# Kernel tuning notes

Measured on AMD Instinct MI355X. Metric: run time of the kernel, lower is better.

The kernel has to match this reference:

```python
import jax, jax.numpy as jnp
import numpy as np

B, N, C, H = 4, 1025, 768, 12
KEEP_RATIO = 0.25
BETA = 1.0


def setup_inputs() -> dict:
    key = jax.random.key(0)
    k1, k2, k3, k4, k5 = jax.random.split(key, 5)
    x = jax.random.normal(k1, (B, N, C), dtype=jnp.float32)
    ucb_count_score = jax.random.uniform(k2, (H, N), dtype=jnp.float32)
    W_qkv = jax.random.normal(k3, (C, 3 * C), dtype=jnp.float32) * 0.02
    W_proj = jax.random.normal(k4, (C, C), dtype=jnp.float32) * 0.02
    b_proj = jax.random.normal(k5, (C,), dtype=jnp.float32) * 0.02
    return {"x": x, "ucb_count_score": ucb_count_score, "W_qkv": W_qkv,
            "W_proj": W_proj, "b_proj": b_proj, "counter": 100, "ucb_enabled": 1}


def reference(x, ucb_count_score, W_qkv, W_proj, b_proj, counter, ucb_enabled):
    Bn, Nn, Cn = x.shape
    Dh = Cn // H
    scale = Dh ** -0.5
    # qkv projection (no bias, qkv_bias=False)
    qkv = (x @ W_qkv).reshape(Bn, Nn, 3, H, Dh)
    q = jnp.transpose(qkv[:, :, 0], (0, 2, 1, 3))  # [B,H,N,Dh]
    k = jnp.transpose(qkv[:, :, 1], (0, 2, 1, 3))
    v = jnp.transpose(qkv[:, :, 2], (0, 2, 1, 3))
    attn_probs = jax.nn.softmax(jnp.einsum('bhnd,bhmd->bhnm', q, k) * scale, axis=-1)

    if ucb_enabled and counter > 50:
        # UCB pruning path (exclude_cls=True, keep_ratio set)
        total_patches = Nn - 1
        k_sel = max(1, int(total_patches * KEEP_RATIO))
        patch_scores = attn_probs[:, :, :, 1:].mean(axis=2)  # [B,H,N-1]
        expl = BETA * jnp.sqrt(jnp.log(counter + 1.0) / (ucb_count_score[:, 1:] + 1e-6))  # [H,N-1]
        global_ucb = (patch_scores + expl[None]).mean(axis=1)  # [B,N-1]
        _, sel = jax.lax.top_k(global_ucb, k_sel)  # [B,k]
        tok = sel + 1  # shift for CLS
        # keep[b,j] = 1 if token j is CLS or selected in batch b
        keep = jnp.zeros((Bn, Nn), dtype=attn_probs.dtype)
        keep = keep.at[jnp.arange(Bn)[:, None], tok].set(1.0).at[:, 0].set(1.0)
        # mask[b,h,i,j] = keep[b,i] OR keep[b,j]
        mask = jnp.maximum(keep[:, None, :, None], keep[:, None, None, :])
        pruned = attn_probs * mask
        pruned = pruned / (pruned.sum(axis=-1, keepdims=True) + 1e-8)
        context = jnp.einsum('bhnm,bhmd->bhnd', pruned, v)
        cnt = jnp.zeros((Nn,), dtype=jnp.float32).at[tok.reshape(-1)].add(1.0) / Bn
        score_delta = jnp.broadcast_to(cnt[None, :], ucb_count_score.shape)
    else:
        context = jnp.einsum('bhnm,bhmd->bhnd', attn_probs, v)
        score_delta = None

    out = context.transpose(0, 2, 1, 3).reshape(Bn, Nn, Cn) @ W_proj + b_proj
    return out, score_delta
```

## Files before the change

### kernel.cpp

```cpp
#include <hip/hip_runtime.h>
#include <hip/hip_bf16.h>
#include <math.h>

#define Bb 4
#define Nn 1025
#define Cc 768
#define Hh 12
#define BH (Bb*Hh)
#define M_ROWS 4100
#define KSEL 256
#define JP 1152
#define IT_TILES 68
#define NIB 17
#define NIB32 33
#define NSW 9
#define MT16 264
#define KC24 24
#define JT16 72
#define JS32 36
#define ESTR 1160
#define NPART 396
#define QSCALE 0.18033688011112042f

typedef __attribute__((ext_vector_type(8))) short short8;
typedef __attribute__((ext_vector_type(4))) float floatx4;

static __device__ inline unsigned short f2bf(float v) {
    __hip_bfloat16 b = __float2bfloat16(v);
    return *reinterpret_cast<unsigned short*>(&b);
}
static __device__ inline unsigned short tbf(float f) {
    union { float f; unsigned u; } x; x.f = f;
    return (unsigned short)(x.u >> 16);
}
static __device__ inline float fexp2(float x) {
    return __builtin_amdgcn_exp2f(x);
}
static __device__ inline float bflo(unsigned u) {
    return __uint_as_float((u & 0xffffu) << 16);
}
static __device__ inline float bfhi(unsigned u) {
    return __uint_as_float(u & 0xffff0000u);
}

static __device__ inline void async16(const unsigned short* g, unsigned short* l) {
    __builtin_amdgcn_global_load_lds(
        (const __attribute__((address_space(1))) unsigned int*)g,
        (__attribute__((address_space(3))) unsigned int*)l, 16, 0, 0);
}

__global__ void zero_ws(unsigned int* p, int n) {
    for (int i = blockIdx.x * 256 + threadIdx.x; i < n; i += gridDim.x * 256)
        p[i] = 0u;
}

__global__ __launch_bounds__(256)
void cast_x(const float* __restrict__ x, unsigned short* __restrict__ xA) {
    int s = blockIdx.x * 256 + threadIdx.x;
    int ml = s & 15, q = (s >> 4) & 3;
    int t2 = s >> 6;
    int mt = t2 % MT16, kc = t2 / MT16;
    int m = mt * 16 + ml, k = kc * 32 + q * 8;
    uint4 pk = {0u, 0u, 0u, 0u};
    if (m < M_ROWS) {
        float4 a = *(const float4*)&x[(size_t)m * 768 + k];
        float4 b2 = *(const float4*)&x[(size_t)m * 768 + k + 4];
        pk.x = (unsigned)f2bf(a.x)  | ((unsigned)f2bf(a.y)  << 16);
        pk.y = (unsigned)f2bf(a.z)  | ((unsigned)f2bf(a.w)  << 16);
        pk.z = (unsigned)f2bf(b2.x) | ((unsigned)f2bf(b2.y) << 16);
        pk.w = (unsigned)f2bf(b2.z) | ((unsigned)f2bf(b2.w) << 16);
    }
    *(uint4*)&xA[(size_t)s * 8] = pk;
}

__global__ __launch_bounds__(256)
void cast_w(const float* __restrict__ W, unsigned short* __restrict__ WB,
            int N, int NT) {
    int s = blockIdx.x * 256 + threadIdx.x;
    int nl = s & 15, q = (s >> 4) & 3;
    int t2 = s >> 6;
    int nt = t2 % NT, kc = t2 / NT;
    int n = nt * 16 + nl, k = kc * 32 + q * 8;
    unsigned hv[8];
#pragma unroll
    for (int e = 0; e < 8; ++e)
        hv[e] = f2bf(W[(size_t)(k + e) * N + n]);
    uint4 pk;
    pk.x = hv[0] | (hv[1] << 16);
    pk.y = hv[2] | (hv[3] << 16);
    pk.z = hv[4] | (hv[5] << 16);
    pk.w = hv[6] | (hv[7] << 16);
    *(uint4*)&WB[(size_t)s * 8] = pk;
}

__global__ __launch_bounds__(256, 2)
void gemm_mfma(const unsigned short* __restrict__ Af,
               const unsigned short* __restrict__ Bf,
               int Nt16, int mode,
               unsigned short* __restrict__ qB, unsigned short* __restrict__ kF,
               unsigned short* __restrict__ vF,
               float* __restrict__ outp, const float* __restrict__ bias)
{
    __shared__ __align__(16) unsigned short ldsA[4096];
    __shared__ __align__(16) unsigned short ldsB[4096];
    const int tid = threadIdx.x;
    const int ln = tid & 63, w = tid >> 6;
    const int wm = w >> 1, wn = w & 1;
    const int mb = blockIdx.x, nb = blockIdx.y;

    floatx4 acc[4][4];
#pragma unroll
    for (int mt = 0; mt < 4; ++mt)
#pragma unroll
        for (int nt = 0; nt < 4; ++nt)
            acc[mt][nt] = (floatx4){0.f, 0.f, 0.f, 0.f};

    for (int kc = 0; kc < KC24; ++kc) {
        const unsigned short* gA = Af + ((size_t)(kc * MT16 + mb * 8)) * 512;
        const unsigned short* gB = Bf + ((size_t)(kc * Nt16 + nb * 8)) * 512;
        async16(gA + (size_t)(w * 128 + ln) * 8,      &ldsA[w * 1024]);
        async16(gA + (size_t)(w * 128 + 64 + ln) * 8, &ldsA[w * 1024 + 512]);
        async16(gB + (size_t)(w * 128 + ln) * 8,      &ldsB[w * 1024]);
        async16(gB + (size_t)(w * 128 + 64 + ln) * 8, &ldsB[w * 1024 + 512]);
        __syncthreads();

        short8 Am[4], Bn[4];
#pragma unroll
        for (int mt = 0; mt < 4; ++mt)
            Am[mt] = *(const short8*)&ldsA[((wm * 4 + mt) * 64 + ln) * 8];
#pragma unroll
        for (int nt = 0; nt < 4; ++nt)
            Bn[nt] = *(const short8*)&ldsB[((wn * 4 + nt) * 64 + ln) * 8];
#pragma unroll
        for (int mt = 0; mt < 4; ++mt)
#pragma unroll
            for (int nt = 0; nt < 4; ++nt)
                acc[mt][nt] = __builtin_amdgcn_mfma_f32_16x16x32_bf16(
                    Am[mt], Bn[nt], acc[mt][nt], 0, 0, 0);
        __syncthreads();
    }

    const int q = ln >> 4, l15 = ln & 15;
    if (mode == 1) {
#pragma unroll
        for (int nt = 0; nt < 4; ++nt) {
            int gn = nb * 128 + wn * 64 + nt * 16 + l15;
            float bv = bias[gn];
#pragma unroll
            for (int mt = 0; mt < 4; ++mt) {
                int gmb = mb * 128 + wm * 64 + mt * 16 + q * 4;
#pragma unroll
                for (int r = 0; r < 4; ++r) {
                    int gm = gmb + r;
                    if (gm < M_ROWS)
                        outp[(size_t)gm * 768 + gn] = acc[mt][nt][r] + bv;
                }
            }
        }
    } else {
#pragma unroll
        for (int nt = 0; nt < 4; ++nt) {
            int gn = nb * 128 + wn * 64 + nt * 16 + l15;
            int s = (gn >= 1536) ? 2 : (gn >= 768 ? 1 : 0);
            int rr = gn - s * Cc;
            int h = rr >> 6, d = rr & 63;
#pragma unroll
            for (int mt = 0; mt < 4; ++mt) {
                int gmb = mb * 128 + wm * 64 + mt * 16 + q * 4;
#pragma unroll
                for (int r = 0; r < 4; ++r) {
                    int gm = gmb + r;
                    if (gm >= M_ROWS) continue;
                    int b = gm / Nn;
                    int n = gm - b * Nn;
                    int bh = b * Hh + h;
                    float val = acc[mt][nt][r];
                    if (s == 0) {
                        int idx = (((bh * IT_TILES + (n >> 4)) * 2 + (d >> 5)) * 512)
                                  + ((((d & 31) >> 3) * 16 + (n & 15)) * 8) + (d & 7);
                        qB[idx] = f2bf(val * QSCALE);
                    } else if (s == 1) {
                        size_t idx = ((((size_t)bh * JT16 + (n >> 4)) * 2 + (d >> 5)) * 64
                                      + ((d >> 3) & 3) * 16 + (n & 15)) * 8 + (d & 7);
                        kF[idx] = f2bf(val);
                    } else {
                        size_t idx = ((((size_t)bh * JS32 + (n >> 5)) * 4 + (d >> 4)) * 64
                                      + ((n >> 3) & 3) * 16 + (d & 15)) * 8 + (n & 7);
                        vF[idx] = f2bf(val);
                    }
                }
            }
        }
    }
}

__global__ __launch_bounds__(256, 2)
void attn_colsum_mfma(const unsigned short* __restrict__ qB,
                      const unsigned short* __restrict__ kF,
                      float* __restrict__ colsum_part)
{
    __shared__ unsigned short expS[32 * ESTR];
    __shared__ float red16[16][32];
    __shared__ float linv[32];

    const int blk = blockIdx.x;
    const int x8 = blk & 7, g = blk >> 3;
    const int bh = x8 * 6 + (g % 6);
    const int ib = g / 6;
    const int tid = threadIdx.x;
    const int ws = tid >> 6;
    const int ln = tid & 63;
    const int i16 = ln & 15, q = ln >> 4;

    const unsigned short* kBase = kF + (size_t)bh * JT16 * 1024;

    short8 Qf[2][2];
#pragma unroll
    for (int it = 0; it < 2; ++it)
#pragma unroll
        for (int kc = 0; kc < 2; ++kc)
            Qf[it][kc] = *(const short8*)&qB[(((size_t)bh * IT_TILES + ib * 2 + it) * 2 + kc) * 512 + ln * 8];

    float lacc[2][2] = {{0.f, 0.f}, {0.f, 0.f}};

    short8 Kc[2][2], Kn[2][2];
#pragma unroll
    for (int jt = 0; jt < 2; ++jt)
#pragma unroll
        for (int kc = 0; kc < 2; ++kc)
            Kc[jt][kc] = *(const short8*)&kBase[(((ws * 2 + jt) * 2 + kc) * 64 + ln) * 8];

    for (int sw = 0; sw < NSW; ++sw) {
        if (sw + 1 < NSW) {
#pragma unroll
            for (int jt = 0; jt < 2; ++jt)
#pragma unroll
                for (int kc = 0; kc < 2; ++kc)
                    Kn[jt][kc] = *(const short8*)&kBase[((((sw + 1) * 8 + ws * 2 + jt) * 2 + kc) * 64 + ln) * 8];
        }

        floatx4 S[2][2];
#pragma unroll
        for (int it = 0; it < 2; ++it)
#pragma unroll
            for (int jt = 0; jt < 2; ++jt) {
                S[it][jt] = (floatx4){0.f, 0.f, 0.f, 0.f};
#pragma unroll
                for (int kc = 0; kc < 2; ++kc)
                    S[it][jt] = __builtin_amdgcn_mfma_f32_16x16x32_bf16(Kc[jt][kc], Qf[it][kc], S[it][jt], 0, 0, 0);
            }

        const int jbase0 = sw * 128 + ws * 32 + q * 4;
#pragma unroll
        for (int it = 0; it < 2; ++it) {
            const int irow = it * 16 + i16;
#pragma unroll
            for (int jt = 0; jt < 2; ++jt) {
                int jbase = jbase0 + jt * 16;
                float p[4];
#pragma unroll
                for (int r = 0; r < 4; ++r) {
                    float vld = (jbase + r < Nn) ? 1.f : 0.f;
                    p[r] = fexp2(S[it][jt][r]) * vld;
                }
                lacc[it][jt] += (p[0] + p[1]) + (p[2] + p[3]);
                uint2 pk;
                pk.x = (unsigned)tbf(p[0]) | ((unsigned)tbf(p[1]) << 16);
                pk.y = (unsigned)tbf(p[2]) | ((unsigned)tbf(p[3]) << 16);
                *(uint2*)&expS[irow * ESTR + jbase] = pk;
            }
        }
#pragma unroll
        for (int jt = 0; jt < 2; ++jt)
#pragma unroll
            for (int kc = 0; kc < 2; ++kc)
                Kc[jt][kc] = Kn[jt][kc];
    }

    __syncthreads();
#pragma unroll
    for (int it = 0; it < 2; ++it)
        red16[ws * 4 + q][it * 16 + i16] = lacc[it][0] + lacc[it][1];
    __syncthreads();
    if (tid < 32) {
        float s = 0.f;
#pragma unroll
        for (int t = 0; t < 16; ++t) s += red16[t][tid];
        int gi = ib * 32 + tid;
        linv[tid] = (gi < Nn) ? 1.f / s : 0.f;
    }
    __syncthreads();

    float* prow = colsum_part + (size_t)(bh * NIB32 + ib) * JP;
    for (int grp = tid; grp < 288; grp += 256) {
        int j0 = grp * 4;
        float a0 = 0.f, a1 = 0.f, a2 = 0.f, a3 = 0.f;
#pragma unroll 8
        for (int i = 0; i < 32; ++i) {
            uint2 v = *(const uint2*)&expS[i * ESTR + j0];
            float li = linv[i];
            a0 += bflo(v.x) * li;
            a1 += bfhi(v.x) * li;
            a2 += bflo(v.y) * li;
            a3 += bfhi(v.y) * li;
        }
        float4 o = {a0, a1, a2, a3};
        *(float4*)&prow[j0] = o;
    }
}

__global__ __launch_bounds__(1024)
void ucb_topk(const float* __restrict__ colsum_part, const float* __restrict__ ucb_score,
              const int* __restrict__ counter_p,
              float* __restrict__ keepP, float* __restrict__ cnt)
{
    const int b = blockIdx.x;
    const int tid = threadIdx.x;
    __shared__ float vals[1024];
    __shared__ int   idxs[1024];

    const int j = tid + 1;
    const float* pb = colsum_part + (size_t)b * NPART * JP + j;
    float c0 = 0.f, c1 = 0.f, c2 = 0.f, c3 = 0.f;
#pragma unroll 4
    for (int g2 = 0; g2 < NPART; g2 += 4) {
        c0 += pb[(size_t)(g2 + 0) * JP];
        c1 += pb[(size_t)(g2 + 1) * JP];
        c2 += pb[(size_t)(g2 + 2) * JP];
        c3 += pb[(size_t)(g2 + 3) * JP];
    }
    float cs = (c0 + c1) + (c2 + c3);

    float lc = logf((float)(*counter_p) + 1.0f);
    float s = cs * (1.0f / (float)Nn);
#pragma unroll
    for (int h = 0; h < Hh; ++h)
        s += sqrtf(lc / (ucb_score[h * Nn + j] + 1e-6f));
    s *= (1.0f / (float)Hh);
    vals[tid] = s; idxs[tid] = tid;
    __syncthreads();

    for (int k = 2; k <= 1024; k <<= 1) {
        for (int jj = k >> 1; jj > 0; jj >>= 1) {
            int partner = tid ^ jj;
            if (partner > tid) {
                float v1 = vals[tid], v2 = vals[partner];
                int i1 = idxs[tid], i2 = idxs[partner];
                bool gt = (v1 > v2) || (v1 == v2 && i1 < i2);
                bool desc = ((tid & k) == 0);
                if (desc ? !gt : gt) {
                    vals[tid] = v2; vals[partner] = v1;
                    idxs[tid] = i2; idxs[partner] = i1;
                }
            }
            __syncthreads();
        }
    }

    if (tid < KSEL) {
        int tok = idxs[tid] + 1;
        keepP[b * JP + tok] = 1.f;
        atomicAdd(&cnt[tok], 1.0f / (float)Bb);
    }
    if (tid == 0) keepP[b * JP + 0] = 1.f;
}

__global__ void write_delta(const float* __restrict__ cnt, float* __restrict__ out2) {
    int t = blockIdx.x * 256 + threadIdx.x;
    if (t < Hh * Nn) out2[t] = cnt[t % Nn];
}

__global__ __launch_bounds__(256, 2)
void attn_ctx_mfma(const unsigned short* __restrict__ qB,
                   const unsigned short* __restrict__ kF,
                   const unsigned short* __restrict__ vF,
                   const float* __restrict__ keepP, unsigned short* __restrict__ ctxA)
{
    __shared__ __align__(16) char smem[29440];
    unsigned short* Pall = (unsigned short*)smem;
    float* red16 = (float*)(smem + 20480);
    float* dinv  = (float*)(smem + 24576);
    float* keeps = (float*)(smem + 24832);
    float* redC  = (float*)smem;

    const int blk = blockIdx.x;
    const int x8 = blk & 7, g = blk >> 3;
    const int bh = x8 * 6 + (g % 6);
    const int ib = g / 6;
    const int b = bh / Hh, h = bh % Hh;
    const int tid = threadIdx.x;
    const int ws = tid >> 6;
    const int ln = tid & 63;
    const int i16 = ln & 15, q = ln >> 4;

    for (int t = tid; t < JP; t += 256) keeps[t] = keepP[b * JP + t];

    const unsigned short* kBase = kF + (size_t)bh * JT16 * 1024;
    const unsigned short* vBase = vF + (size_t)bh * JS32 * 2048;

    short8 Qf[4][2];
#pragma unroll
    for (int it = 0; it < 4; ++it)
#pragma unroll
        for (int kc = 0; kc < 2; ++kc)
            Qf[it][kc] = *(const short8*)&qB[(((size_t)bh * IT_TILES + ib * 4 + it) * 2 + kc) * 512 + ln * 8];

    __syncthreads();

    float keepi[4];
#pragma unroll
    for (int it = 0; it < 4; ++it)
        keepi[it] = keeps[(ib * 4 + it) * 16 + i16];

    floatx4 ctxacc[4][4];
#pragma unroll
    for (int it = 0; it < 4; ++it)
#pragma unroll
        for (int dt = 0; dt < 4; ++dt)
            ctxacc[it][dt] = (floatx4){0.f, 0.f, 0.f, 0.f};
    float dsacc[4] = {0.f, 0.f, 0.f, 0.f};

    unsigned short* Pw = Pall + ws * 2560;

    short8 Kc[2][2], Kn[2][2], Vc[4], Vn[4];
#pragma unroll
    for (int jt = 0; jt < 2; ++jt)
#pragma unroll
        for (int kc = 0; kc < 2; ++kc)
            Kc[jt][kc] = *(const short8*)&kBase[(((ws * 2 + jt) * 2 + kc) * 64 + ln) * 8];
#pragma unroll
    for (int dt = 0; dt < 4; ++dt)
        Vc[dt] = *(const short8*)&vBase[((ws * 4 + dt) * 64 + ln) * 8];

    for (int sw = 0; sw < NSW; ++sw) {
        if (sw + 1 < NSW) {
#pragma unroll
            for (int jt = 0; jt < 2; ++jt)
#pragma unroll
                for (int kc = 0; kc < 2; ++kc)
                    Kn[jt][kc] = *(const short8*)&kBase[((((sw + 1) * 8 + ws * 2 + jt) * 2 + kc) * 64 + ln) * 8];
#pragma unroll
            for (int dt = 0; dt < 4; ++dt)
                Vn[dt] = *(const short8*)&vBase[((((sw + 1) * 4 + ws) * 4 + dt) * 64 + ln) * 8];
        }

        float kjv[2][4], vld[2][4];
#pragma unroll
        for (int jt = 0; jt < 2; ++jt)
#pragma unroll
            for (int r = 0; r < 4; ++r) {
                int jj = sw * 128 + ws * 32 + jt * 16 + q * 4 + r;
                vld[jt][r] = (jj < Nn) ? 1.f : 0.f;
                kjv[jt][r] = keeps[jj];
            }

#pragma unroll
        for (int it = 0; it < 4; ++it) {
            floatx4 S[2];
#pragma unroll
            for (int jt = 0; jt < 2; ++jt) {
                S[jt] = (floatx4){0.f, 0.f, 0.f, 0.f};
#pragma unroll
                for (int kc = 0; kc < 2; ++kc)
                    S[jt] = __builtin_amdgcn_mfma_f32_16x16x32_bf16(Kc[jt][kc], Qf[it][kc], S[jt], 0, 0, 0);
            }
            bool rk = keepi[it] > 0.5f;
#pragma unroll
            for (int jt = 0; jt < 2; ++jt) {
                float p[4];
#pragma unroll
                for (int r = 0; r < 4; ++r) {
                    float w = rk ? vld[jt][r] : kjv[jt][r];
                    p[r] = fexp2(S[jt][r]) * w;
                    dsacc[it] += p[r];
                }
                unsigned int lo = (unsigned)tbf(p[0]) | ((unsigned)tbf(p[1]) << 16);
                unsigned int hi = (unsigned)tbf(p[2]) | ((unsigned)tbf(p[3]) << 16);
                uint2 pk; pk.x = lo; pk.y = hi;
                *(uint2*)&Pw[(it * 16 + i16) * 40 + jt * 16 + q * 4] = pk;
            }
        }

        short8 Pf[4];
#pragma unroll
        for (int it = 0; it < 4; ++it)
            Pf[it] = *(const short8*)&Pw[(it * 16 + i16) * 40 + q * 8];
#pragma unroll
        for (int it = 0; it < 4; ++it)
#pragma unroll
            for (int dt = 0; dt < 4; ++dt)
                ctxacc[it][dt] = __builtin_amdgcn_mfma_f32_16x16x32_bf16(Pf[it], Vc[dt], ctxacc[it][dt], 0, 0, 0);

#pragma unroll
        for (int jt = 0; jt < 2; ++jt)
#pragma unroll
            for (int kc = 0; kc < 2; ++kc)
                Kc[jt][kc] = Kn[jt][kc];
#pragma unroll
        for (int dt = 0; dt < 4; ++dt)
            Vc[dt] = Vn[dt];
    }

    __syncthreads();
#pragma unroll
    for (int it = 0; it < 4; ++it) red16[(ws * 4 + q) * 64 + it * 16 + i16] = dsacc[it];
    __syncthreads();
    if (tid < 64) {
        float s = 0.f;
#pragma unroll
        for (int t = 0; t < 16; ++t) s += red16[t * 64 + tid];
        dinv[tid] = 1.f / (s + 1e-8f);
    }
    for (int w = 0; w < 4; ++w) {
        __syncthreads();
        if (ws == w) {
#pragma unroll
            for (int it = 0; it < 4; ++it)
#pragma unroll
                for (int dt = 0; dt < 4; ++dt)
#pragma unroll
                    for (int r = 0; r < 4; ++r) {
                        int i = it * 16 + q * 4 + r;
                        int d = dt * 16 + i16;
                        float v = ctxacc[it][dt][r];
                        redC[i * 66 + d] = (w == 0) ? v : (redC[i * 66 + d] + v);
                    }
        }
    }
    __syncthreads();
#pragma unroll
    for (int rep = 0; rep < 2; ++rep) {
        int s2 = tid + rep * 256;
        int i = s2 >> 3, dc = s2 & 7;
        int gi = ib * 64 + i;
        if (gi < Nn) {
            int m = b * Nn + gi;
            float dv = dinv[i];
            const float* src = &redC[i * 66 + dc * 8];
            uint4 pk;
            pk.x = (unsigned)f2bf(src[0] * dv) | ((unsigned)f2bf(src[1] * dv) << 16);
            pk.y = (unsigned)f2bf(src[2] * dv) | ((unsigned)f2bf(src[3] * dv) << 16);
            pk.z = (unsigned)f2bf(src[4] * dv) | ((unsigned)f2bf(src[5] * dv) << 16);
            pk.w = (unsigned)f2bf(src[6] * dv) | ((unsigned)f2bf(src[7] * dv) << 16);
            int kc2 = h * 2 + (dc >> 2);
            int q2 = dc & 3;
            size_t idx = (((size_t)(kc2 * MT16 + (m >> 4))) * 64 + q2 * 16 + (m & 15)) * 8;
            *(uint4*)&ctxA[idx] = pk;
        }
    }
}

extern "C" void kernel_launch(void* const* d_in, const int* in_sizes, int n_in,
                              void* d_out, int out_size, void* d_ws, size_t ws_size,
                              hipStream_t stream) {
    const float* x     = (const float*)d_in[0];
    const float* ucb   = (const float*)d_in[1];
    const float* Wqkv  = (const float*)d_in[2];
    const float* Wproj = (const float*)d_in[3];
    const float* bproj = (const float*)d_in[4];
    const int*   counter = (const int*)d_in[5];

    unsigned short* qB = (unsigned short*)d_ws;
    unsigned short* kF = qB + 3342336;
    unsigned short* vF = kF + 3538944;
    float* colsum_b = (float*)(vF + 3538944);
    float* keepP    = colsum_b + 4608;
    float* cnt      = keepP + 4608;
    unsigned short* ctxA = (unsigned short*)(cnt + 1152);
    unsigned short* xA   = ctxA + 3244032;
    unsigned short* WB   = xA + 3244032;
    unsigned short* WpB  = WB + 1769472;
    float* colsum_part = (float*)(WpB + 589824);

    float* out  = (float*)d_out;
    float* out2 = out + 3148800;

    zero_ws<<<dim3(2048), dim3(256), 0, stream>>>((unsigned int*)d_ws, 5220480);
    cast_x<<<dim3(1584), dim3(256), 0, stream>>>(x, xA);
    cast_w<<<dim3(864), dim3(256), 0, stream>>>(Wqkv, WB, 2304, 144);
    cast_w<<<dim3(288), dim3(256), 0, stream>>>(Wproj, WpB, 768, 48);

    gemm_mfma<<<dim3(33, 18), dim3(256), 0, stream>>>(
        xA, WB, 144, 0, qB, kF, vF, nullptr, nullptr);
    attn_colsum_mfma<<<dim3(8 * 198), dim3(256), 0, stream>>>(qB, kF, colsum_part);
    ucb_topk<<<dim3(Bb), dim3(1024), 0, stream>>>(colsum_part, ucb, counter, keepP, cnt);
    write_delta<<<dim3(49), dim3(256), 0, stream>>>(cnt, out2);
    attn_ctx_mfma<<<dim3(8 * 102), dim3(256), 0, stream>>>(qB, kF, vF, keepP, ctxA);
    gemm_mfma<<<dim3(33, 6), dim3(256), 0, stream>>>(
        ctxA, WpB, 48, 1, nullptr, nullptr, nullptr, out, bproj);
}
```

Baseline: 237.8 us.

## Merge cast kernels, drop workspace zeroing, fold delta write into attention

Merges the three cast kernels into one launch and removes the full-workspace zeroing kernel. The top-k kernel now clears its own keep and per-batch count buffers, which replaces atomics with plain per-batch writes. The score-delta output is written inside the attention-context kernel, so the write_delta launch goes away. Launch bounds on attention-context rise to 3 blocks per SM, which may add register pressure. The intent is to cut launch count and the cost of zeroing about 20MB of workspace.

```diff
diff --git a/kernel.cpp b/kernel.cpp
--- a/kernel.cpp
+++ b/kernel.cpp
@@ -22,6 +22,10 @@
 #define NPART 396
 #define QSCALE 0.18033688011112042f
 
+#define CAST_X_BLK 1584
+#define CAST_WQKV_BLK 864
+#define CAST_WPROJ_BLK 288
+
 typedef __attribute__((ext_vector_type(8))) short short8;
 typedef __attribute__((ext_vector_type(4))) float floatx4;
 
@@ -49,34 +53,42 @@
         (__attribute__((address_space(3))) unsigned int*)l, 16, 0, 0);
 }
 
-__global__ void zero_ws(unsigned int* p, int n) {
-    for (int i = blockIdx.x * 256 + threadIdx.x; i < n; i += gridDim.x * 256)
-        p[i] = 0u;
-}
-
 __global__ __launch_bounds__(256)
-void cast_x(const float* __restrict__ x, unsigned short* __restrict__ xA) {
-    int s = blockIdx.x * 256 + threadIdx.x;
-    int ml = s & 15, q = (s >> 4) & 3;
-    int t2 = s >> 6;
-    int mt = t2 % MT16, kc = t2 / MT16;
-    int m = mt * 16 + ml, k = kc * 32 + q * 8;
-    uint4 pk = {0u, 0u, 0u, 0u};
-    if (m < M_ROWS) {
-        float4 a = *(const float4*)&x[(size_t)m * 768 + k];
-        float4 b2 = *(const float4*)&x[(size_t)m * 768 + k + 4];
-        pk.x = (unsigned)f2bf(a.x)  | ((unsigned)f2bf(a.y)  << 16);
-        pk.y = (unsigned)f2bf(a.z)  | ((unsigned)f2bf(a.w)  << 16);
-        pk.z = (unsigned)f2bf(b2.x) | ((unsigned)f2bf(b2.y) << 16);
-        pk.w = (unsigned)f2bf(b2.z) | ((unsigned)f2bf(b2.w) << 16);
-    }
-    *(uint4*)&xA[(size_t)s * 8] = pk;
-}
-
-__global__ __launch_bounds__(256)
-void cast_w(const float* __restrict__ W, unsigned short* __restrict__ WB,
-            int N, int NT) {
-    int s = blockIdx.x * 256 + threadIdx.x;
+void cast_all(const float* __restrict__ x, const float* __restrict__ Wqkv,
+              const float* __restrict__ Wproj,
+              unsigned short* __restrict__ xA, unsigned short* __restrict__ WB,
+              unsigned short* __restrict__ WpB)
+{
+    int blk = blockIdx.x;
+    int tid = threadIdx.x;
+    if (blk < CAST_X_BLK) {
+        int s = blk * 256 + tid;
+        int ml = s & 15, q = (s >> 4) & 3;
+        int t2 = s >> 6;
+        int mt = t2 % MT16, kc = t2 / MT16;
+        int m = mt * 16 + ml, k = kc * 32 + q * 8;
+        uint4 pk = {0u, 0u, 0u, 0u};
+        if (m < M_ROWS) {
+            float4 a = *(const float4*)&x[(size_t)m * 768 + k];
+            float4 b2 = *(const float4*)&x[(size_t)m * 768 + k + 4];
+            pk.x = (unsigned)f2bf(a.x)  | ((unsigned)f2bf(a.y)  << 16);
+            pk.y = (unsigned)f2bf(a.z)  | ((unsigned)f2bf(a.w)  << 16);
+            pk.z = (unsigned)f2bf(b2.x) | ((unsigned)f2bf(b2.y) << 16);
+            pk.w = (unsigned)f2bf(b2.z) | ((unsigned)f2bf(b2.w) << 16);
+        }
+        *(uint4*)&xA[(size_t)s * 8] = pk;
+        return;
+    }
+    const float* W;
+    unsigned short* WO;
+    int N, NT, s;
+    if (blk < CAST_X_BLK + CAST_WQKV_BLK) {
+        W = Wqkv; WO = WB; N = 2304; NT = 144;
+        s = (blk - CAST_X_BLK) * 256 + tid;
+    } else {
+        W = Wproj; WO = WpB; N = 768; NT = 48;
+        s = (blk - CAST_X_BLK - CAST_WQKV_BLK) * 256 + tid;
+    }
     int nl = s & 15, q = (s >> 4) & 3;
     int t2 = s >> 6;
     int nt = t2 % NT, kc = t2 / NT;
@@ -90,7 +102,7 @@
     pk.y = hv[2] | (hv[3] << 16);
     pk.z = hv[4] | (hv[5] << 16);
     pk.w = hv[6] | (hv[7] << 16);
-    *(uint4*)&WB[(size_t)s * 8] = pk;
+    *(uint4*)&WO[(size_t)s * 8] = pk;
 }
 
 __global__ __launch_bounds__(256, 2)
@@ -312,12 +324,17 @@
 __global__ __launch_bounds__(1024)
 void ucb_topk(const float* __restrict__ colsum_part, const float* __restrict__ ucb_score,
               const int* __restrict__ counter_p,
-              float* __restrict__ keepP, float* __restrict__ cnt)
+              float* __restrict__ keepP, float* __restrict__ cnt_b)
 {
     const int b = blockIdx.x;
     const int tid = threadIdx.x;
     __shared__ float vals[1024];
     __shared__ int   idxs[1024];
+
+    for (int t = tid; t < JP; t += 1024) {
+        keepP[b * JP + t] = 0.f;
+        cnt_b[b * JP + t] = 0.f;
+    }
 
     const int j = tid + 1;
     const float* pb = colsum_part + (size_t)b * NPART * JP + j;
@@ -360,21 +377,17 @@
     if (tid < KSEL) {
         int tok = idxs[tid] + 1;
         keepP[b * JP + tok] = 1.f;
-        atomicAdd(&cnt[tok], 1.0f / (float)Bb);
+        cnt_b[b * JP + tok] = 1.0f / (float)Bb;
     }
     if (tid == 0) keepP[b * JP + 0] = 1.f;
 }
 
-__global__ void write_delta(const float* __restrict__ cnt, float* __restrict__ out2) {
-    int t = blockIdx.x * 256 + threadIdx.x;
-    if (t < Hh * Nn) out2[t] = cnt[t % Nn];
-}
-
-__global__ __launch_bounds__(256, 2)
+__global__ __launch_bounds__(256, 3)
 void attn_ctx_mfma(const unsigned short* __restrict__ qB,
                    const unsigned short* __restrict__ kF,
                    const unsigned short* __restrict__ vF,
-                   const float* __restrict__ keepP, unsigned short* __restrict__ ctxA)
+                   const float* __restrict__ keepP, const float* __restrict__ cnt_b,
+                   unsigned short* __restrict__ ctxA, float* __restrict__ out2)
 {
     __shared__ __align__(16) char smem[29440];
     unsigned short* Pall = (unsigned short*)smem;
@@ -392,6 +405,15 @@
     const int ws = tid >> 6;
     const int ln = tid & 63;
     const int i16 = ln & 15, q = ln >> 4;
+
+    {
+        int t = blk * 256 + tid;
+        if (t < Hh * Nn) {
+            int n = t % Nn;
+            out2[t] = cnt_b[0 * JP + n] + cnt_b[1 * JP + n]
+                    + cnt_b[2 * JP + n] + cnt_b[3 * JP + n];
+        }
+    }
 
     for (int t = tid; t < JP; t += 256) keeps[t] = keepP[b * JP + t];
 
@@ -563,10 +585,9 @@
     unsigned short* qB = (unsigned short*)d_ws;
     unsigned short* kF = qB + 3342336;
     unsigned short* vF = kF + 3538944;
-    float* colsum_b = (float*)(vF + 3538944);
-    float* keepP    = colsum_b + 4608;
-    float* cnt      = keepP + 4608;
-    unsigned short* ctxA = (unsigned short*)(cnt + 1152);
+    float* keepP    = (float*)(vF + 3538944);
+    float* cnt_b    = keepP + 4608;
+    unsigned short* ctxA = (unsigned short*)(cnt_b + 4608);
     unsigned short* xA   = ctxA + 3244032;
     unsigned short* WB   = xA + 3244032;
     unsigned short* WpB  = WB + 1769472;
@@ -575,17 +596,13 @@
     float* out  = (float*)d_out;
     float* out2 = out + 3148800;
 
-    zero_ws<<<dim3(2048), dim3(256), 0, stream>>>((unsigned int*)d_ws, 5220480);
-    cast_x<<<dim3(1584), dim3(256), 0, stream>>>(x, xA);
-    cast_w<<<dim3(864), dim3(256), 0, stream>>>(Wqkv, WB, 2304, 144);
-    cast_w<<<dim3(288), dim3(256), 0, stream>>>(Wproj, WpB, 768, 48);
-
+    cast_all<<<dim3(CAST_X_BLK + CAST_WQKV_BLK + CAST_WPROJ_BLK), dim3(256), 0, stream>>>(
+        x, Wqkv, Wproj, xA, WB, WpB);
     gemm_mfma<<<dim3(33, 18), dim3(256), 0, stream>>>(
         xA, WB, 144, 0, qB, kF, vF, nullptr, nullptr);
     attn_colsum_mfma<<<dim3(8 * 198), dim3(256), 0, stream>>>(qB, kF, colsum_part);
-    ucb_topk<<<dim3(Bb), dim3(1024), 0, stream>>>(colsum_part, ucb, counter, keepP, cnt);
-    write_delta<<<dim3(49), dim3(256), 0, stream>>>(cnt, out2);
-    attn_ctx_mfma<<<dim3(8 * 102), dim3(256), 0, stream>>>(qB, kF, vF, keepP, ctxA);
+    ucb_topk<<<dim3(Bb), dim3(1024), 0, stream>>>(colsum_part, ucb, counter, keepP, cnt_b);
+    attn_ctx_mfma<<<dim3(8 * 102), dim3(256), 0, stream>>>(qB, kF, vF, keepP, cnt_b, ctxA, out2);
     gemm_mfma<<<dim3(33, 6), dim3(256), 0, stream>>>(
         ctxA, WpB, 48, 1, nullptr, nullptr, nullptr, out, bproj);
 }
```

Result: slower. 297.2 us (+25.0%).
